# Optimization experiments

Hardware: AMD Instinct MI355X
Metric: run time of the kernel (lower is better)

The kernel has to match this reference:

```python
import jax, jax.numpy as jnp
import numpy as np
import math

L_MAX = 4
R_BINS = 16
R_MAX = 8.0
VOXEL = 0.5


def _precompute_basis():
    # grid: n = floor(2*r_max/voxel)+1 points per axis, g = n^3
    n = int(math.floor(2 * R_MAX / VOXEL)) + 1
    xs = np.linspace(-R_MAX, R_MAX, n)
    X, Y, Z = np.meshgrid(xs, xs, xs, indexing='ij')
    xyz = np.stack([X, Y, Z], -1).reshape(-1, 3)
    r = np.maximum(np.sqrt((xyz ** 2).sum(-1)), 1e-12)
    ct = np.clip(xyz[:, 2] / r, -1.0, 1.0)           # cos(theta)
    phi = np.arctan2(xyz[:, 1], xyz[:, 0])
    G = xyz.shape[0]
    L = L_MAX
    st = np.sqrt(np.maximum(0.0, 1.0 - ct ** 2))     # sin(theta)
    # associated Legendre P_l^m(cos theta) with Condon-Shortley phase
    P = np.zeros((L + 1, L + 1, G))
    P[0, 0] = 1.0
    for m in range(1, L + 1):
        P[m, m] = -(2 * m - 1) * st * P[m - 1, m - 1]
    for m in range(L):
        P[m + 1, m] = (2 * m + 1) * ct * P[m, m]
    for m in range(L + 1):
        for l in range(m + 2, L + 1):
            P[l, m] = ((2 * l - 1) * ct * P[l - 1, m] - (l + m - 1) * P[l - 2, m]) / (l - m)
    # real spherical harmonics, 'component' normalization (= sqrt(4pi) * orthonormal real SH),
    # packed centered on the m axis: column index L_MAX + m  (mirrors split_Y_by_l_centered)
    Mmax = 2 * L + 1
    Ylmg = np.zeros((L + 1, Mmax, G))
    for l in range(L + 1):
        for m in range(0, l + 1):
            norm = math.sqrt((2 * l + 1) * math.factorial(l - m) / math.factorial(l + m))
            base = norm * P[l, m]
            if m == 0:
                Ylmg[l, L] = base
            else:
                Ylmg[l, L + m] = math.sqrt(2.0) * base * np.cos(m * phi)
                Ylmg[l, L - m] = math.sqrt(2.0) * base * np.sin(m * phi)
    # radial Gaussian RBF (make_radial_rbf), transposed to [R, G]
    edges = np.linspace(0.0, R_MAX, R_BINS + 1)
    centers = 0.5 * (edges[:-1] + edges[1:])
    sigma = (edges[1] - edges[0]) * 0.5
    Rbf = np.exp(-0.5 * ((r[:, None] - centers) / (sigma + 1e-12)) ** 2).T
    return Ylmg.astype(np.float32), Rbf.astype(np.float32)


def setup_inputs() -> dict:
    key = jax.random.key(0)
    Y_lmg, Rbf = _precompute_basis()               # [5,9,35937], [16,35937]
    coeffs = jax.random.normal(key, (2, 32, 4, L_MAX + 1, 2 * L_MAX + 1, R_BINS), dtype=jnp.float32)
    return {"coeffs": coeffs, "Y_lmg": jnp.asarray(Y_lmg), "Rbf": jnp.asarray(Rbf)}


def reference(coeffs, Y_lmg, Rbf):
    # fused equivalent of torch.einsum('bnclmr,lmg,rg->bncg', coeffs, Y_lmg, Rbf)
    # contraction order chosen to avoid the huge (b,n,c,r,g) intermediate:
    basis = jnp.einsum('lmg,rg->lmrg', Y_lmg, Rbf)          # [5,9,16,G] ~103MB
    density = jnp.einsum('bnclmr,lmrg->bncg', coeffs, basis)
    return density.astype(jnp.float16)
```

## Files before the change

### kernel.cpp

```cpp
#include <hip/hip_runtime.h>


#define G_TOTAL 35937
#define N_ROWS  256

typedef __attribute__((ext_vector_type(8))) short bf16x8;
typedef __attribute__((ext_vector_type(16))) float f32x16;

__constant__ int c_lmFlat[25] = {4, 12,13,14, 20,21,22,23,24,
                                 28,29,30,31,32,33,34,
                                 36,37,38,39,40,41,42,43,44};

__global__ __launch_bounds__(256, 3) void sh_fused(
        const float* __restrict__ coeffs,
        const float* __restrict__ Y,
        const float* __restrict__ Rb,
        float* __restrict__ out) {
    __shared__ uint4 Alds[25 * 64];
    const int tx = threadIdx.x;
    const int l  = tx & 63;
    const int w  = tx >> 6;
    const int cl = l & 31;
    const int kg = l >> 5;

    const int mt = blockIdx.y;
    const int g0 = blockIdx.x * 256 + w * 64 + cl;
    const int g1 = g0 + 32;
    const int gc0 = g0 < G_TOTAL ? g0 : G_TOTAL - 1;
    const int gc1 = g1 < G_TOTAL ? g1 : G_TOTAL - 1;

#pragma unroll
    for (int i = 0; i < 4; ++i) {
        int c = tx + i * 256;
        if (c < 800) {
            int ks  = c >> 5;
            int r32 = c & 31;
            const float4* src = (const float4*)(coeffs + (mt * 32 + r32) * 720
                                                + c_lmFlat[ks] * 16);
            float4 f0 = src[0], f1 = src[1], f2 = src[2], f3 = src[3];
            unsigned u0, u1, u2, u3, u4, u5, u6, u7;
            asm("v_cvt_pk_bf16_f32 %0, %1, %2" : "=v"(u0) : "v"(f0.x), "v"(f0.y));
            asm("v_cvt_pk_bf16_f32 %0, %1, %2" : "=v"(u1) : "v"(f0.z), "v"(f0.w));
            asm("v_cvt_pk_bf16_f32 %0, %1, %2" : "=v"(u2) : "v"(f1.x), "v"(f1.y));
            asm("v_cvt_pk_bf16_f32 %0, %1, %2" : "=v"(u3) : "v"(f1.z), "v"(f1.w));
            asm("v_cvt_pk_bf16_f32 %0, %1, %2" : "=v"(u4) : "v"(f2.x), "v"(f2.y));
            asm("v_cvt_pk_bf16_f32 %0, %1, %2" : "=v"(u5) : "v"(f2.z), "v"(f2.w));
            asm("v_cvt_pk_bf16_f32 %0, %1, %2" : "=v"(u6) : "v"(f3.x), "v"(f3.y));
            asm("v_cvt_pk_bf16_f32 %0, %1, %2" : "=v"(u7) : "v"(f3.z), "v"(f3.w));
            Alds[ks * 64 + r32]      = make_uint4(u0, u1, u2, u3);
            Alds[ks * 64 + 32 + r32] = make_uint4(u4, u5, u6, u7);
        }
    }

    constexpr int lmFlat[25] = {4, 12,13,14, 20,21,22,23,24,
                                28,29,30,31,32,33,34,
                                36,37,38,39,40,41,42,43,44};
    float YA[25], YB[25];
#pragma unroll
    for (int i = 0; i < 25; ++i) {
        YA[i] = Y[lmFlat[i] * G_TOTAL + gc0];
        YB[i] = Y[lmFlat[i] * G_TOTAL + gc1];
    }
    float RA[8], RB[8];
#pragma unroll
    for (int j = 0; j < 8; ++j) {
        RA[j] = Rb[(kg * 8 + j) * G_TOTAL + gc0];
        RB[j] = Rb[(kg * 8 + j) * G_TOTAL + gc1];
    }

    f32x16 acc0, acc1;
#pragma unroll
    for (int q = 0; q < 16; ++q) { acc0[q] = 0.0f; acc1[q] = 0.0f; }

    __syncthreads();

    const bf16x8* __restrict__ Al = (const bf16x8*)Alds;
#pragma unroll
    for (int ks = 0; ks < 25; ++ks) {
        const float y0 = YA[ks];
        const float y1 = YB[ks];
        union { unsigned int u[4]; bf16x8 v; } fb0, fb1;
#pragma unroll
        for (int p = 0; p < 4; ++p) {
            float a_lo = y0 * RA[2 * p], a_hi = y0 * RA[2 * p + 1];
            float b_lo = y1 * RB[2 * p], b_hi = y1 * RB[2 * p + 1];
            unsigned ra, rb;
            asm("v_cvt_pk_bf16_f32 %0, %1, %2" : "=v"(ra) : "v"(a_lo), "v"(a_hi));
            asm("v_cvt_pk_bf16_f32 %0, %1, %2" : "=v"(rb) : "v"(b_lo), "v"(b_hi));
            fb0.u[p] = ra;
            fb1.u[p] = rb;
        }
        bf16x8 a = Al[ks * 64 + l];
        acc0 = __builtin_amdgcn_mfma_f32_32x32x16_bf16(a, fb0.v, acc0, 0, 0, 0);
        acc1 = __builtin_amdgcn_mfma_f32_32x32x16_bf16(a, fb1.v, acc1, 0, 0, 0);
    }

    const int rbase = mt * 32 + 4 * kg;
    if (g0 < G_TOTAL) {
#pragma unroll
        for (int reg = 0; reg < 16; ++reg) {
            int ro = (reg & 3) + 8 * (reg >> 2);
            out[(rbase + ro) * G_TOTAL + g0] = acc0[reg];
        }
    }
    if (g1 < G_TOTAL) {
#pragma unroll
        for (int reg = 0; reg < 16; ++reg) {
            int ro = (reg & 3) + 8 * (reg >> 2);
            out[(rbase + ro) * G_TOTAL + g1] = acc1[reg];
        }
    }
}

extern "C" void kernel_launch(void* const* d_in, const int* in_sizes, int n_in,
                              void* d_out, int out_size, void* d_ws, size_t ws_size,
                              hipStream_t stream) {
    const float *pC = nullptr, *pY = nullptr, *pR = nullptr;
    if (n_in >= 3) {
        for (int i = 0; i < 3; ++i) {
            if      (in_sizes[i] == 256 * 720)    pC = (const float*)d_in[i];
            else if (in_sizes[i] == 45 * G_TOTAL) pY = (const float*)d_in[i];
            else if (in_sizes[i] == 16 * G_TOTAL) pR = (const float*)d_in[i];
        }
    }
    if (!pC || !pY || !pR) {
        pC = (const float*)d_in[0];
        pY = (const float*)d_in[1];
        pR = (const float*)d_in[2];
    }

    float* out = (float*)d_out;

    dim3 grid(141, 8);
    sh_fused<<<grid, 256, 0, stream>>>(pC, pY, pR, out);

    (void)d_ws; (void)ws_size; (void)out_size; (void)n_in;
}
```

Measured before the change: 25.34 us.

## Remap blocks so same-column tiles share an XCD and stage Y via LDS

Launches a 1D grid with a manual block remap so the 8 row tiles (mt) of one g-column chunk are issued to the same XCD, letting them share Y/Rbf reads in that XCD's L2. Y values are loaded cooperatively into shared memory with float4 loads instead of 50 scalar per-thread global loads held in registers. This is meant to cut redundant L2/HBM traffic and register pressure. In exchange it adds extra LDS usage, some idle early-exit blocks, and LDS reads inside the MFMA loop.

Result: no change. 25.58 us (+0.9%).

```diff
diff --git a/kernel.cpp b/kernel.cpp
--- a/kernel.cpp
+++ b/kernel.cpp
@@ -2,7 +2,7 @@
 
 
 #define G_TOTAL 35937
-#define N_ROWS  256
+#define NCS 141
 
 typedef __attribute__((ext_vector_type(8))) short bf16x8;
 typedef __attribute__((ext_vector_type(16))) float f32x16;
@@ -17,17 +17,30 @@
         const float* __restrict__ Rb,
         float* __restrict__ out) {
     __shared__ uint4 Alds[25 * 64];
+    __shared__ float Ylds[25 * 256];
+
+    const int bid = blockIdx.x;
+    const int xcd = bid & 7;
+    const int r   = bid >> 3;
+    const int cs  = xcd + 8 * (r >> 3);
+    const int mt  = r & 7;
+    if (cs >= NCS) return;
+
     const int tx = threadIdx.x;
     const int l  = tx & 63;
     const int w  = tx >> 6;
     const int cl = l & 31;
     const int kg = l >> 5;
 
-    const int mt = blockIdx.y;
-    const int g0 = blockIdx.x * 256 + w * 64 + cl;
+    const int gbase = cs * 256;
+    const int g0 = gbase + w * 64 + cl;
     const int g1 = g0 + 32;
     const int gc0 = g0 < G_TOTAL ? g0 : G_TOTAL - 1;
     const int gc1 = g1 < G_TOTAL ? g1 : G_TOTAL - 1;
+
+    constexpr int lmFlat[25] = {4, 12,13,14, 20,21,22,23,24,
+                                28,29,30,31,32,33,34,
+                                36,37,38,39,40,41,42,43,44};
 
 #pragma unroll
     for (int i = 0; i < 4; ++i) {
@@ -36,7 +49,7 @@
             int ks  = c >> 5;
             int r32 = c & 31;
             const float4* src = (const float4*)(coeffs + (mt * 32 + r32) * 720
-                                                + c_lmFlat[ks] * 16);
+                                                + lmFlat[ks] * 16);
             float4 f0 = src[0], f1 = src[1], f2 = src[2], f3 = src[3];
             unsigned u0, u1, u2, u3, u4, u5, u6, u7;
             asm("v_cvt_pk_bf16_f32 %0, %1, %2" : "=v"(u0) : "v"(f0.x), "v"(f0.y));
@@ -52,15 +65,25 @@
         }
     }
 
-    constexpr int lmFlat[25] = {4, 12,13,14, 20,21,22,23,24,
-                                28,29,30,31,32,33,34,
-                                36,37,38,39,40,41,42,43,44};
-    float YA[25], YB[25];
+    if (gbase + 256 <= G_TOTAL) {
 #pragma unroll
-    for (int i = 0; i < 25; ++i) {
-        YA[i] = Y[lmFlat[i] * G_TOTAL + gc0];
-        YB[i] = Y[lmFlat[i] * G_TOTAL + gc1];
+        for (int i = 0; i < 7; ++i) {
+            int c = tx + i * 256;
+            if (c < 1600) {
+                int row = c >> 6;
+                int c4  = c & 63;
+                float4 v = *(const float4*)(Y + lmFlat[row] * G_TOTAL + gbase + c4 * 4);
+                *(float4*)(Ylds + row * 256 + c4 * 4) = v;
+            }
+        }
+    } else {
+        int gcl = gbase + tx;
+        if (gcl > G_TOTAL - 1) gcl = G_TOTAL - 1;
+#pragma unroll
+        for (int row = 0; row < 25; ++row)
+            Ylds[row * 256 + tx] = Y[lmFlat[row] * G_TOTAL + gcl];
     }
+
     float RA[8], RB[8];
 #pragma unroll
     for (int j = 0; j < 8; ++j) {
@@ -77,8 +100,8 @@
     const bf16x8* __restrict__ Al = (const bf16x8*)Alds;
 #pragma unroll
     for (int ks = 0; ks < 25; ++ks) {
-        const float y0 = YA[ks];
-        const float y1 = YB[ks];
+        const float y0 = Ylds[ks * 256 + w * 64 + cl];
+        const float y1 = Ylds[ks * 256 + w * 64 + 32 + cl];
         union { unsigned int u[4]; bf16x8 v; } fb0, fb1;
 #pragma unroll
         for (int p = 0; p < 4; ++p) {
@@ -131,8 +154,7 @@
 
     float* out = (float*)d_out;
 
-    dim3 grid(141, 8);
-    sh_fused<<<grid, 256, 0, stream>>>(pC, pY, pR, out);
+    sh_fused<<<1152, 256, 0, stream>>>(pC, pY, pR, out);
 
     (void)d_ws; (void)ws_size; (void)out_size; (void)n_in;
 }
```
